# Performance work log

Measured on AMD Instinct MI355X. Metric: run time of the kernel, lower is better.

Reference implementation:

```python
import jax, jax.numpy as jnp
import numpy as np
import math

B, N = 2, 384
TF, POS, TIME = 22, 32, 32
TPROJ = TIME + 1  # embed_fixed appends frame_mask channel
CS, CZ = 256, 128
POS_MAX, TIME_MAX = 2056.0, 10000.0
LN_EPS = 1e-5


def _index_emb(idx):
    # sinusoidal positional embedding of integer indices -> [..., POS]
    K = jnp.arange(POS // 2, dtype=jnp.float32)
    ang = idx[..., None].astype(jnp.float32) * jnp.pi / (POS_MAX ** (2.0 * K / POS))
    return jnp.concatenate([jnp.sin(ang), jnp.cos(ang)], axis=-1)


def _time_emb(t):
    # standard score-sde timestep embedding -> [M, TIME]
    half = TIME // 2
    freqs = jnp.exp(-(math.log(TIME_MAX) / (half - 1)) * jnp.arange(half, dtype=jnp.float32))
    ang = t[:, None] * freqs[None, :]
    return jnp.concatenate([jnp.sin(ang), jnp.cos(ang)], axis=-1)


def _ln(x, g, b):
    m = jnp.mean(x, axis=-1, keepdims=True)
    v = jnp.var(x, axis=-1, keepdims=True)
    return (x - m) * jax.lax.rsqrt(v + LN_EPS) * g + b


def _lin(x, W, b):
    return x @ W.T + b


def _forward(seq_idx, seq_feat, timestep, frame_mask,
             W_npos, b_npos, W_ntf, b_ntf, W_ntime, b_ntime,
             W_n1, b_n1, W_n2, b_n2, g_n, be_n,
             W_epos, b_epos, W_etf, b_etf, W_etime, b_etime,
             W_e1, b_e1, W_e2, b_e2, g_e, be_e):
    Bn, Nn = seq_idx.shape
    rel = seq_idx[:, :, None] - seq_idx[:, None, :]  # [B,N,N]
    seq_emb = _lin(_index_emb(seq_idx), W_npos, b_npos)          # [B,N,CS]
    edge_emb = _lin(_index_emb(rel), W_epos, b_epos)             # [B,N,N,CZ]
    seq_emb = seq_emb + _lin(seq_feat, W_ntf, b_ntf)
    # _cross_concat(x) @ W^T == (x @ Wl^T)[:, :, None] + (x @ Wr^T)[:, None, :] + b
    # (same math, avoids the O(N^2 * 2*TF) concatenated intermediate)
    edge_emb = edge_emb + (seq_feat @ W_etf[:, :TF].T)[:, :, None, :] \
                        + (seq_feat @ W_etf[:, TF:].T)[:, None, :, :] + b_etf
    t_res = (timestep[:, None] * frame_mask).reshape(-1)
    temb = _time_emb(t_res).reshape(Bn, Nn, TIME)
    temb = jnp.concatenate([temb, frame_mask[..., None]], axis=-1)  # embed_fixed -> TPROJ
    seq_emb = seq_emb + _lin(temb, W_ntime, b_ntime)
    edge_emb = edge_emb + (temb @ W_etime[:, :TPROJ].T)[:, :, None, :] \
                        + (temb @ W_etime[:, TPROJ:].T)[:, None, :, :] + b_etime
    # node_embedder: ReLU -> Linear -> ReLU -> Linear -> LayerNorm
    h = _lin(jax.nn.relu(seq_emb), W_n1, b_n1)
    seq_emb = _ln(_lin(jax.nn.relu(h), W_n2, b_n2), g_n, be_n)
    h = _lin(jax.nn.relu(edge_emb), W_e1, b_e1)
    edge_emb = _ln(_lin(jax.nn.relu(h), W_e2, b_e2), g_e, be_e)
    return seq_emb, edge_emb


def setup_inputs() -> dict:
    key = jax.random.key(0)
    ks = jax.random.split(key, 20)
    inp = {
        'seq_idx': jnp.sort(jax.random.randint(ks[0], (B, N), 0, 1000), axis=-1),
        'seq_feat': jax.random.normal(ks[1], (B, N, TF), dtype=jnp.float32),
        'timestep': jax.random.uniform(ks[2], (B,), dtype=jnp.float32),
        'frame_mask': jnp.ones((B, N), dtype=jnp.float32),
    }
    def lin(k, o, i):
        return 0.02 * jax.random.normal(k, (o, i), dtype=jnp.float32), jnp.zeros((o,), jnp.float32)
    inp['W_npos'], inp['b_npos'] = lin(ks[3], CS, POS)
    inp['W_ntf'], inp['b_ntf'] = lin(ks[4], CS, TF)
    inp['W_ntime'], inp['b_ntime'] = lin(ks[5], CS, TPROJ)
    inp['W_n1'], inp['b_n1'] = lin(ks[6], CS, CS)
    inp['W_n2'], inp['b_n2'] = lin(ks[7], CS, CS)
    inp['g_n'], inp['be_n'] = jnp.ones((CS,), jnp.float32), jnp.zeros((CS,), jnp.float32)
    inp['W_epos'], inp['b_epos'] = lin(ks[8], CZ, POS)
    inp['W_etf'], inp['b_etf'] = lin(ks[9], CZ, 2 * TF)
    inp['W_etime'], inp['b_etime'] = lin(ks[10], CZ, 2 * TPROJ)
    inp['W_e1'], inp['b_e1'] = lin(ks[11], CZ, CZ)
    inp['W_e2'], inp['b_e2'] = lin(ks[12], CZ, CZ)
    inp['g_e'], inp['be_e'] = jnp.ones((CZ,), jnp.float32), jnp.zeros((CZ,), jnp.float32)
    return inp


def reference(seq_idx, seq_feat, timestep, frame_mask,
              W_npos, b_npos, W_ntf, b_ntf, W_ntime, b_ntime,
              W_n1, b_n1, W_n2, b_n2, g_n, be_n,
              W_epos, b_epos, W_etf, b_etf, W_etime, b_etime,
              W_e1, b_e1, W_e2, b_e2, g_e, be_e):
    return _forward(seq_idx, seq_feat, timestep, frame_mask,
                    W_npos, b_npos, W_ntf, b_ntf, W_ntime, b_ntime,
                    W_n1, b_n1, W_n2, b_n2, g_n, be_n,
                    W_epos, b_epos, W_etf, b_etf, W_etime, b_etime,
                    W_e1, b_e1, W_e2, b_e2, g_e, be_e)
```

## Files before the change

### kernel.cpp

```cpp
#include <hip/hip_runtime.h>
#include <hip/hip_bf16.h>

#define BB 2
#define NN 384
#define TFD 22
#define POSD 32
#define TPROJ 33
#define CS 256
#define CZ 128
#define PI_F 3.14159265358979323846f

typedef __hip_bfloat16 bf16;
typedef __attribute__((ext_vector_type(8))) short short8;
typedef __attribute__((ext_vector_type(4))) short short4v;
typedef __attribute__((ext_vector_type(4))) float floatx4;

__device__ __forceinline__ float bfbits2f(unsigned short u) {
  unsigned v = ((unsigned)u) << 16;
  float f;
  __builtin_memcpy(&f, &v, 4);
  return f;
}
__device__ __forceinline__ unsigned short f2bf(float x) {
  bf16 h = __float2bfloat16(x);
  unsigned short u;
  __builtin_memcpy(&u, &h, 2);
  return u;
}
__device__ __forceinline__ bool probe_f32(const void* fm) {
  return *(const unsigned*)fm == 0x3F800000u;
}
__device__ __forceinline__ float ldf(const void* p, int j, bool f32) {
  return f32 ? ((const float*)p)[j] : bfbits2f(((const unsigned short*)p)[j]);
}

#define TAB_OFF 0
#define SEQ0_OFF 262144
#define EL_OFF 458752
#define ER_OFF 557056
#define P2_OFF 655360
#define WB_OFF 656896
#define qBN1 0
#define qBN2 256
#define qGN 512
#define qBEN 768
#define qBE1 1024
#define qBE2 1152
#define qGE 1280
#define qBEE 1408
#define UB_WE1 0
#define UB_WE2 16384
#define UB_WN1 32768
#define UB_WN2 98304

#define NODE8_BLKS 96
#define TAB_BLKS 1024
#define CVT_BLKS 646
#define NODE_BLKS 48

struct InPtrs { const void* p[28]; };

__global__ __launch_bounds__(256) void prep(InPtrs ip, const int* __restrict__ seq_idx,
                                            float* __restrict__ ws) {
  const bool f32 = probe_f32(ip.p[3]);
  const int blk = blockIdx.x;
  const int t = threadIdx.x;
  if (blk < NODE8_BLKS) {
    __shared__ float feat[8][88];
    const int bn0 = blk * 8;
    if (t < 128) {
      const int n = t >> 4, j = t & 15, bn = bn0 + n, b = bn / NN;
      const float fm = ldf(ip.p[3], bn, f32);
      const float idxv = (float)seq_idx[bn];
      const float ang = idxv * PI_F * powf(2056.0f, -(float)j * (1.0f / 16.0f));
      feat[n][j] = sinf(ang);
      feat[n][16 + j] = cosf(ang);
      const float tres = ldf(ip.p[2], b, f32) * fm;
      const float freq = expf(-(logf(10000.0f) * (1.0f / 15.0f)) * (float)j);
      feat[n][54 + j] = sinf(tres * freq);
      feat[n][70 + j] = cosf(tres * freq);
      if (j == 0) feat[n][86] = fm;
    }
    if (t < 176) {
      const int n = t / TFD, j = t - n * TFD;
      feat[n][32 + j] = ldf(ip.p[1], (bn0 + n) * TFD + j, f32);
    }
    __syncthreads();
    {
      const int c = t;
      const float bias = ldf(ip.p[5], c, f32) + ldf(ip.p[7], c, f32) + ldf(ip.p[9], c, f32);
      float acc[8];
#pragma unroll
      for (int n = 0; n < 8; ++n) acc[n] = bias;
      if (f32) {
        const float* w = (const float*)ip.p[4] + c * POSD;
#pragma unroll
        for (int k = 0; k < POSD; ++k) { const float wv = w[k];
#pragma unroll
          for (int n = 0; n < 8; ++n) acc[n] += feat[n][k] * wv; }
        const float* w2 = (const float*)ip.p[6] + c * TFD;
#pragma unroll
        for (int k = 0; k < TFD; ++k) { const float wv = w2[k];
#pragma unroll
          for (int n = 0; n < 8; ++n) acc[n] += feat[n][32 + k] * wv; }
        const float* w3 = (const float*)ip.p[8] + c * TPROJ;
#pragma unroll
        for (int k = 0; k < TPROJ; ++k) { const float wv = w3[k];
#pragma unroll
          for (int n = 0; n < 8; ++n) acc[n] += feat[n][54 + k] * wv; }
      } else {
        const unsigned short* w = (const unsigned short*)ip.p[4] + c * POSD;
#pragma unroll
        for (int k = 0; k < POSD; ++k) { const float wv = bfbits2f(w[k]);
#pragma unroll
          for (int n = 0; n < 8; ++n) acc[n] += feat[n][k] * wv; }
        const unsigned short* w2 = (const unsigned short*)ip.p[6] + c * TFD;
#pragma unroll
        for (int k = 0; k < TFD; ++k) { const float wv = bfbits2f(w2[k]);
#pragma unroll
          for (int n = 0; n < 8; ++n) acc[n] += feat[n][32 + k] * wv; }
        const unsigned short* w3 = (const unsigned short*)ip.p[8] + c * TPROJ;
#pragma unroll
        for (int k = 0; k < TPROJ; ++k) { const float wv = bfbits2f(w3[k]);
#pragma unroll
          for (int n = 0; n < 8; ++n) acc[n] += feat[n][54 + k] * wv; }
      }
#pragma unroll
      for (int n = 0; n < 8; ++n) ws[SEQ0_OFF + (bn0 + n) * CS + c] = acc[n];
    }
    {
      const int isR = t >> 7;
      const int c = t & 127;
      const int o1 = isR ? TFD : 0, o2 = isR ? TPROJ : 0;
      const int dst = isR ? ER_OFF : EL_OFF;
      float acc[8];
#pragma unroll
      for (int n = 0; n < 8; ++n) acc[n] = 0.0f;
      if (f32) {
        const float* w = (const float*)ip.p[18] + c * (2 * TFD) + o1;
#pragma unroll
        for (int k = 0; k < TFD; ++k) { const float wv = w[k];
#pragma unroll
          for (int n = 0; n < 8; ++n) acc[n] += feat[n][32 + k] * wv; }
        const float* w2 = (const float*)ip.p[20] + c * (2 * TPROJ) + o2;
#pragma unroll
        for (int k = 0; k < TPROJ; ++k) { const float wv = w2[k];
#pragma unroll
          for (int n = 0; n < 8; ++n) acc[n] += feat[n][54 + k] * wv; }
      } else {
        const unsigned short* w = (const unsigned short*)ip.p[18] + c * (2 * TFD) + o1;
#pragma unroll
        for (int k = 0; k < TFD; ++k) { const float wv = bfbits2f(w[k]);
#pragma unroll
          for (int n = 0; n < 8; ++n) acc[n] += feat[n][32 + k] * wv; }
        const unsigned short* w2 = (const unsigned short*)ip.p[20] + c * (2 * TPROJ) + o2;
#pragma unroll
        for (int k = 0; k < TPROJ; ++k) { const float wv = bfbits2f(w2[k]);
#pragma unroll
          for (int n = 0; n < 8; ++n) acc[n] += feat[n][54 + k] * wv; }
      }
#pragma unroll
      for (int n = 0; n < 8; ++n) ws[dst + (bn0 + n) * CZ + c] = acc[n];
    }
  } else if (blk < NODE8_BLKS + TAB_BLKS) {
    __shared__ float spe[2][POSD];
    const int r0 = (blk - NODE8_BLKS) * 2;
    const int rr = t >> 7, c = t & 127;
    if (c < 16) {
      float ang = (float)(r0 + rr - 1024) * PI_F * powf(2056.0f, -(float)c * (1.0f / 16.0f));
      spe[rr][c] = sinf(ang);
      spe[rr][c + 16] = cosf(ang);
    }
    __syncthreads();
    float acc = ldf(ip.p[17], c, f32) + ldf(ip.p[19], c, f32) + ldf(ip.p[21], c, f32);
    if (f32) {
      const float* w = (const float*)ip.p[16] + c * POSD;
#pragma unroll
      for (int k = 0; k < POSD; ++k) acc += spe[rr][k] * w[k];
    } else {
      const unsigned short* w = (const unsigned short*)ip.p[16] + c * POSD;
#pragma unroll
      for (int k = 0; k < POSD; ++k) acc += spe[rr][k] * bfbits2f(w[k]);
    }
    ws[TAB_OFF + (r0 + rr) * CZ + c] = acc;
  } else {
    const int idx = (blk - NODE8_BLKS - TAB_BLKS) * 256 + t;
    if (idx < 1536) {
      int src, off;
      if (idx < 256)       { src = 11; off = idx; }
      else if (idx < 512)  { src = 13; off = idx - 256; }
      else if (idx < 768)  { src = 14; off = idx - 512; }
      else if (idx < 1024) { src = 15; off = idx - 768; }
      else if (idx < 1152) { src = 23; off = idx - 1024; }
      else if (idx < 1280) { src = 25; off = idx - 1152; }
      else if (idx < 1408) { src = 26; off = idx - 1280; }
      else                 { src = 27; off = idx - 1408; }
      ws[P2_OFF + idx] = ldf(ip.p[src], off, f32);
    } else {
      const int j = idx - 1536;
      int src, loc;
      if (j < 16384)      { src = 22; loc = j; }
      else if (j < 32768) { src = 24; loc = j - 16384; }
      else if (j < 98304) { src = 10; loc = j - 32768; }
      else                { src = 12; loc = j - 98304; }
      const void* sp = ip.p[src];
      unsigned short* wb = (unsigned short*)(ws + WB_OFF);
      wb[j] = f32 ? f2bf(((const float*)sp)[loc]) : ((const unsigned short*)sp)[loc];
    }
  }
}

union SMem {
  struct {
    unsigned short A0[32][CZ + 8];
    unsigned short A1[32][CZ + 8];
    float O[32][CZ + 4];
    int J[NN];
  } e;
  struct {
    unsigned short A0[16][CS + 8];
    unsigned short A1[16][CS + 8];
    float O[16][CS + 4];
    float Red[16][16];
    float RedQ[16][16];
    float Mu[16];
    float Rs[16];
  } n;
};

__global__ __launch_bounds__(256) void main_mfma(const int* __restrict__ seq_idx,
                                                 const float* __restrict__ ws,
                                                 const void* __restrict__ fmraw,
                                                 void* __restrict__ outv) {
  __shared__ __align__(16) SMem sm;
  const int t = threadIdx.x;
  const int wave = t >> 6, lane = t & 63, quad = lane >> 4, l16 = lane & 15;
  const float* P2 = ws + P2_OFF;
  const unsigned short* WB = (const unsigned short*)(ws + WB_OFF);
  const bool f32o = probe_f32(fmraw);

  if (blockIdx.x < NODE_BLKS) {
    const int row0 = blockIdx.x * 16;
    const unsigned short* W1 = WB + UB_WN1;
    const unsigned short* W2 = WB + UB_WN2;
    const float* seq0 = ws + SEQ0_OFF;
#pragma unroll
    for (int r = 0; r < 16; ++r)
      sm.n.A0[r][t] = f2bf(fmaxf(seq0[(row0 + r) * CS + t], 0.0f));
    __syncthreads();
    short8 af[8];
    floatx4 acc[4];
#pragma unroll
    for (int ks = 0; ks < 8; ++ks) af[ks] = *(const short8*)&sm.n.A0[l16][ks * 32 + quad * 8];
#pragma unroll
    for (int n = 0; n < 4; ++n) acc[n] = (floatx4){0.f, 0.f, 0.f, 0.f};
#pragma unroll
    for (int ntl = 0; ntl < 4; ++ntl) {
      const int n0 = wave * 64 + ntl * 16;
#pragma unroll
      for (int ks = 0; ks < 8; ++ks) {
        short8 bfr = *(const short8*)&W1[(n0 + l16) * CS + ks * 32 + quad * 8];
        acc[ntl] = __builtin_amdgcn_mfma_f32_16x16x32_bf16(af[ks], bfr, acc[ntl], 0, 0, 0);
      }
    }
#pragma unroll
    for (int ntl = 0; ntl < 4; ++ntl) {
      const int n0 = wave * 64 + ntl * 16;
      const float b1v = P2[qBN1 + n0 + l16];
#pragma unroll
      for (int i = 0; i < 4; ++i)
        sm.n.A1[quad * 4 + i][n0 + l16] = f2bf(fmaxf(acc[ntl][i] + b1v, 0.0f));
    }
    __syncthreads();
#pragma unroll
    for (int ks = 0; ks < 8; ++ks) af[ks] = *(const short8*)&sm.n.A1[l16][ks * 32 + quad * 8];
#pragma unroll
    for (int n = 0; n < 4; ++n) acc[n] = (floatx4){0.f, 0.f, 0.f, 0.f};
#pragma unroll
    for (int ntl = 0; ntl < 4; ++ntl) {
      const int n0 = wave * 64 + ntl * 16;
#pragma unroll
      for (int ks = 0; ks < 8; ++ks) {
        short8 bfr = *(const short8*)&W2[(n0 + l16) * CS + ks * 32 + quad * 8];
        acc[ntl] = __builtin_amdgcn_mfma_f32_16x16x32_bf16(af[ks], bfr, acc[ntl], 0, 0, 0);
      }
    }
#pragma unroll
    for (int ntl = 0; ntl < 4; ++ntl) {
      const int n0 = wave * 64 + ntl * 16;
      const float b2v = P2[qBN2 + n0 + l16];
#pragma unroll
      for (int i = 0; i < 4; ++i)
        sm.n.O[quad * 4 + i][n0 + l16] = acc[ntl][i] + b2v;
    }
    __syncthreads();
    {
      const int r = t >> 4, seg = t & 15;
      float s = 0.f, q = 0.f;
#pragma unroll
      for (int k = 0; k < 16; ++k) { float v = sm.n.O[r][seg * 16 + k]; s += v; q += v * v; }
      sm.n.Red[r][seg] = s;
      sm.n.RedQ[r][seg] = q;
    }
    __syncthreads();
    if (t < 16) {
      float s = 0.f, q = 0.f;
#pragma unroll
      for (int k = 0; k < 16; ++k) { s += sm.n.Red[t][k]; q += sm.n.RedQ[t][k]; }
      float mu = s * (1.0f / CS);
      float var = q * (1.0f / CS) - mu * mu;
      sm.n.Mu[t] = mu;
      sm.n.Rs[t] = rsqrtf(var + 1e-5f);
    }
    __syncthreads();
    {
      const float g = P2[qGN + t], be = P2[qBEN + t];
      if (f32o) {
        float* o = (float*)outv;
#pragma unroll
        for (int r = 0; r < 16; ++r)
          o[(size_t)(row0 + r) * CS + t] = (sm.n.O[r][t] - sm.n.Mu[r]) * sm.n.Rs[r] * g + be;
      } else {
        bf16* o = (bf16*)outv;
#pragma unroll
        for (int r = 0; r < 16; ++r)
          o[(size_t)(row0 + r) * CS + t] =
              __float2bfloat16((sm.n.O[r][t] - sm.n.Mu[r]) * sm.n.Rs[r] * g + be);
      }
    }
    return;
  }

  const int eb = blockIdx.x - NODE_BLKS;
  const int irow = eb % NN, b = eb / NN;
  const unsigned short* W1 = WB + UB_WE1;
  const unsigned short* W2 = WB + UB_WE2;
  const float* tab = ws + TAB_OFF;
  const float* eL = ws + EL_OFF;
  const float* eR = ws + ER_OFF;
  short8 w1f[2][4], w2f[2][4];
  float b1v[2], b2v[2];
#pragma unroll
  for (int ntl = 0; ntl < 2; ++ntl) {
    const int n0 = (wave * 2 + ntl) * 16;
    b1v[ntl] = P2[qBE1 + n0 + l16];
    b2v[ntl] = P2[qBE2 + n0 + l16];
#pragma unroll
    for (int ks = 0; ks < 4; ++ks) {
      w1f[ntl][ks] = *(const short8*)&W1[(n0 + l16) * CZ + ks * 32 + quad * 8];
      w2f[ntl][ks] = *(const short8*)&W2[(n0 + l16) * CZ + ks * 32 + quad * 8];
    }
  }
  for (int k = t; k < NN; k += 256) sm.e.J[k] = seq_idx[b * NN + k];
  const int idx_i = seq_idx[b * NN + irow];
  const int c4 = (t & 31) * 4;
  const int rg = t >> 5;
  const floatx4 eLv = *(const floatx4*)&eL[(b * NN + irow) * CZ + c4];
  const int lr = t >> 3, lseg = t & 7;
  const size_t base0 = ((size_t)(b * NN + irow) * NN) * CZ;
  __syncthreads();

  for (int jt = 0; jt < NN / 32; ++jt) {
    const int j0 = jt * 32;
#pragma unroll
    for (int rr = 0; rr < 4; ++rr) {
      const int r = rg + rr * 8;
      int rel = idx_i - sm.e.J[j0 + r] + 1024;
      rel = min(max(rel, 0), 2047);
      const floatx4 tv = *(const floatx4*)&tab[rel * CZ + c4];
      const floatx4 ev = *(const floatx4*)&eR[(b * NN + j0 + r) * CZ + c4];
      short4v sv;
      sv[0] = (short)f2bf(fmaxf(tv[0] + ev[0] + eLv[0], 0.0f));
      sv[1] = (short)f2bf(fmaxf(tv[1] + ev[1] + eLv[1], 0.0f));
      sv[2] = (short)f2bf(fmaxf(tv[2] + ev[2] + eLv[2], 0.0f));
      sv[3] = (short)f2bf(fmaxf(tv[3] + ev[3] + eLv[3], 0.0f));
      *(short4v*)&sm.e.A0[r][c4] = sv;
    }
    __syncthreads();
    short8 af[2][4];
    floatx4 acc[2][2];
#pragma unroll
    for (int mt = 0; mt < 2; ++mt)
#pragma unroll
      for (int ks = 0; ks < 4; ++ks)
        af[mt][ks] = *(const short8*)&sm.e.A0[mt * 16 + l16][ks * 32 + quad * 8];
#pragma unroll
    for (int mt = 0; mt < 2; ++mt)
#pragma unroll
      for (int n = 0; n < 2; ++n) acc[mt][n] = (floatx4){0.f, 0.f, 0.f, 0.f};
#pragma unroll
    for (int ntl = 0; ntl < 2; ++ntl)
#pragma unroll
      for (int ks = 0; ks < 4; ++ks) {
        acc[0][ntl] = __builtin_amdgcn_mfma_f32_16x16x32_bf16(af[0][ks], w1f[ntl][ks], acc[0][ntl], 0, 0, 0);
        acc[1][ntl] = __builtin_amdgcn_mfma_f32_16x16x32_bf16(af[1][ks], w1f[ntl][ks], acc[1][ntl], 0, 0, 0);
      }
#pragma unroll
    for (int ntl = 0; ntl < 2; ++ntl) {
      const int n0 = (wave * 2 + ntl) * 16;
#pragma unroll
      for (int mt = 0; mt < 2; ++mt)
#pragma unroll
        for (int i = 0; i < 4; ++i)
          sm.e.A1[mt * 16 + quad * 4 + i][n0 + l16] = f2bf(fmaxf(acc[mt][ntl][i] + b1v[ntl], 0.0f));
    }
    __syncthreads();
#pragma unroll
    for (int mt = 0; mt < 2; ++mt)
#pragma unroll
      for (int ks = 0; ks < 4; ++ks)
        af[mt][ks] = *(const short8*)&sm.e.A1[mt * 16 + l16][ks * 32 + quad * 8];
#pragma unroll
    for (int mt = 0; mt < 2; ++mt)
#pragma unroll
      for (int n = 0; n < 2; ++n) acc[mt][n] = (floatx4){0.f, 0.f, 0.f, 0.f};
#pragma unroll
    for (int ntl = 0; ntl < 2; ++ntl)
#pragma unroll
      for (int ks = 0; ks < 4; ++ks) {
        acc[0][ntl] = __builtin_amdgcn_mfma_f32_16x16x32_bf16(af[0][ks], w2f[ntl][ks], acc[0][ntl], 0, 0, 0);
        acc[1][ntl] = __builtin_amdgcn_mfma_f32_16x16x32_bf16(af[1][ks], w2f[ntl][ks], acc[1][ntl], 0, 0, 0);
      }
#pragma unroll
    for (int ntl = 0; ntl < 2; ++ntl) {
      const int n0 = (wave * 2 + ntl) * 16;
#pragma unroll
      for (int mt = 0; mt < 2; ++mt)
#pragma unroll
        for (int i = 0; i < 4; ++i)
          sm.e.O[mt * 16 + quad * 4 + i][n0 + l16] = acc[mt][ntl][i] + b2v[ntl];
    }
    __syncthreads();
    {
      float s = 0.f, q = 0.f;
      float vals[16];
#pragma unroll
      for (int k = 0; k < 16; ++k) {
        const float v = sm.e.O[lr][lseg * 16 + k];
        vals[k] = v;
        s += v;
        q += v * v;
      }
      s += __shfl_xor(s, 1); q += __shfl_xor(q, 1);
      s += __shfl_xor(s, 2); q += __shfl_xor(q, 2);
      s += __shfl_xor(s, 4); q += __shfl_xor(q, 4);
      const float mu = s * (1.0f / CZ);
      const float rs = rsqrtf(q * (1.0f / CZ) - mu * mu + 1e-5f);
      const int cbase = lseg * 16;
      const size_t obase = base0 + (size_t)(j0 + lr) * CZ + cbase;
      if (f32o) {
        float* o = (float*)outv + (size_t)BB * NN * CS;
#pragma unroll
        for (int h = 0; h < 4; ++h) {
          const floatx4 gq = *(const floatx4*)&P2[qGE + cbase + h * 4];
          const floatx4 bq = *(const floatx4*)&P2[qBEE + cbase + h * 4];
          floatx4 ov;
#pragma unroll
          for (int i = 0; i < 4; ++i) ov[i] = (vals[h * 4 + i] - mu) * rs * gq[i] + bq[i];
          *(floatx4*)&o[obase + h * 4] = ov;
        }
      } else {
        bf16* o = (bf16*)outv + (size_t)BB * NN * CS;
        short8 pk[2];
#pragma unroll
        for (int h = 0; h < 4; ++h) {
          const floatx4 gq = *(const floatx4*)&P2[qGE + cbase + h * 4];
          const floatx4 bq = *(const floatx4*)&P2[qBEE + cbase + h * 4];
#pragma unroll
          for (int i = 0; i < 4; ++i)
            pk[h >> 1][(h & 1) * 4 + i] = (short)f2bf((vals[h * 4 + i] - mu) * rs * gq[i] + bq[i]);
        }
        *(short8*)&o[obase] = pk[0];
        *(short8*)&o[obase + 8] = pk[1];
      }
    }
  }
}

extern "C" void kernel_launch(void* const* d_in, const int* in_sizes, int n_in,
                              void* d_out, int out_size, void* d_ws, size_t ws_size,
                              hipStream_t stream) {
  (void)in_sizes; (void)n_in; (void)out_size; (void)ws_size;
  const int* seq_idx = (const int*)d_in[0];
  float* ws = (float*)d_ws;
  InPtrs ip;
  for (int i = 0; i < 28; ++i) ip.p[i] = d_in[i];
  hipLaunchKernelGGL(prep, dim3(NODE8_BLKS + TAB_BLKS + CVT_BLKS), dim3(256), 0, stream,
                     ip, seq_idx, ws);
  hipLaunchKernelGGL(main_mfma, dim3(NODE_BLKS + BB * NN), dim3(256), 0, stream,
                     seq_idx, ws, d_in[3], d_out);
}
```

Before: 310.5 us.

## Split node/edge kernels and make edge MLP wave-private with register-built A tiles

Splits the combined kernel into a node kernel and a separate edge kernel launch. In the edge kernel each wave now owns its own 32 rows and covers all 128 output columns, so the block-wide syncthreads and shared staging disappear. The ReLU input tiles are built straight into MFMA registers, the hidden activation goes through a small XOR-swizzled per-wave LDS scratch, and LayerNorm is done with in-register shuffles. In exchange, weights are reloaded from global or L2 for every tile instead of kept in registers. Output stores become scalar strided writes rather than 16-byte vectors, and register pressure rises with 16 accumulators.

```diff
diff --git a/kernel.cpp b/kernel.cpp
--- a/kernel.cpp
+++ b/kernel.cpp
@@ -12,7 +12,6 @@
 
 typedef __hip_bfloat16 bf16;
 typedef __attribute__((ext_vector_type(8))) short short8;
-typedef __attribute__((ext_vector_type(4))) short short4v;
 typedef __attribute__((ext_vector_type(4))) float floatx4;
 
 __device__ __forceinline__ float bfbits2f(unsigned short u) {
@@ -210,268 +209,265 @@
   }
 }
 
-union SMem {
-  struct {
-    unsigned short A0[32][CZ + 8];
-    unsigned short A1[32][CZ + 8];
-    float O[32][CZ + 4];
-    int J[NN];
-  } e;
-  struct {
-    unsigned short A0[16][CS + 8];
-    unsigned short A1[16][CS + 8];
-    float O[16][CS + 4];
-    float Red[16][16];
-    float RedQ[16][16];
-    float Mu[16];
-    float Rs[16];
-  } n;
+struct SMemN {
+  unsigned short A0[16][CS + 8];
+  unsigned short A1[16][CS + 8];
+  float O[16][CS + 4];
+  float Red[16][16];
+  float RedQ[16][16];
+  float Mu[16];
+  float Rs[16];
 };
 
-__global__ __launch_bounds__(256) void main_mfma(const int* __restrict__ seq_idx,
-                                                 const float* __restrict__ ws,
+__global__ __launch_bounds__(256) void node_mfma(const float* __restrict__ ws,
                                                  const void* __restrict__ fmraw,
                                                  void* __restrict__ outv) {
-  __shared__ __align__(16) SMem sm;
+  __shared__ __align__(16) SMemN sm;
   const int t = threadIdx.x;
   const int wave = t >> 6, lane = t & 63, quad = lane >> 4, l16 = lane & 15;
   const float* P2 = ws + P2_OFF;
   const unsigned short* WB = (const unsigned short*)(ws + WB_OFF);
   const bool f32o = probe_f32(fmraw);
-
-  if (blockIdx.x < NODE_BLKS) {
-    const int row0 = blockIdx.x * 16;
-    const unsigned short* W1 = WB + UB_WN1;
-    const unsigned short* W2 = WB + UB_WN2;
-    const float* seq0 = ws + SEQ0_OFF;
-#pragma unroll
-    for (int r = 0; r < 16; ++r)
-      sm.n.A0[r][t] = f2bf(fmaxf(seq0[(row0 + r) * CS + t], 0.0f));
-    __syncthreads();
-    short8 af[8];
-    floatx4 acc[4];
-#pragma unroll
-    for (int ks = 0; ks < 8; ++ks) af[ks] = *(const short8*)&sm.n.A0[l16][ks * 32 + quad * 8];
-#pragma unroll
-    for (int n = 0; n < 4; ++n) acc[n] = (floatx4){0.f, 0.f, 0.f, 0.f};
-#pragma unroll
-    for (int ntl = 0; ntl < 4; ++ntl) {
-      const int n0 = wave * 64 + ntl * 16;
-#pragma unroll
-      for (int ks = 0; ks < 8; ++ks) {
-        short8 bfr = *(const short8*)&W1[(n0 + l16) * CS + ks * 32 + quad * 8];
-        acc[ntl] = __builtin_amdgcn_mfma_f32_16x16x32_bf16(af[ks], bfr, acc[ntl], 0, 0, 0);
-      }
-    }
-#pragma unroll
-    for (int ntl = 0; ntl < 4; ++ntl) {
-      const int n0 = wave * 64 + ntl * 16;
-      const float b1v = P2[qBN1 + n0 + l16];
-#pragma unroll
-      for (int i = 0; i < 4; ++i)
-        sm.n.A1[quad * 4 + i][n0 + l16] = f2bf(fmaxf(acc[ntl][i] + b1v, 0.0f));
-    }
-    __syncthreads();
-#pragma unroll
-    for (int ks = 0; ks < 8; ++ks) af[ks] = *(const short8*)&sm.n.A1[l16][ks * 32 + quad * 8];
-#pragma unroll
-    for (int n = 0; n < 4; ++n) acc[n] = (floatx4){0.f, 0.f, 0.f, 0.f};
-#pragma unroll
-    for (int ntl = 0; ntl < 4; ++ntl) {
-      const int n0 = wave * 64 + ntl * 16;
-#pragma unroll
-      for (int ks = 0; ks < 8; ++ks) {
-        short8 bfr = *(const short8*)&W2[(n0 + l16) * CS + ks * 32 + quad * 8];
-        acc[ntl] = __builtin_amdgcn_mfma_f32_16x16x32_bf16(af[ks], bfr, acc[ntl], 0, 0, 0);
-      }
-    }
-#pragma unroll
-    for (int ntl = 0; ntl < 4; ++ntl) {
-      const int n0 = wave * 64 + ntl * 16;
-      const float b2v = P2[qBN2 + n0 + l16];
-#pragma unroll
-      for (int i = 0; i < 4; ++i)
-        sm.n.O[quad * 4 + i][n0 + l16] = acc[ntl][i] + b2v;
-    }
-    __syncthreads();
-    {
-      const int r = t >> 4, seg = t & 15;
-      float s = 0.f, q = 0.f;
-#pragma unroll
-      for (int k = 0; k < 16; ++k) { float v = sm.n.O[r][seg * 16 + k]; s += v; q += v * v; }
-      sm.n.Red[r][seg] = s;
-      sm.n.RedQ[r][seg] = q;
-    }
-    __syncthreads();
-    if (t < 16) {
-      float s = 0.f, q = 0.f;
-#pragma unroll
-      for (int k = 0; k < 16; ++k) { s += sm.n.Red[t][k]; q += sm.n.RedQ[t][k]; }
-      float mu = s * (1.0f / CS);
-      float var = q * (1.0f / CS) - mu * mu;
-      sm.n.Mu[t] = mu;
-      sm.n.Rs[t] = rsqrtf(var + 1e-5f);
-    }
-    __syncthreads();
-    {
-      const float g = P2[qGN + t], be = P2[qBEN + t];
-      if (f32o) {
-        float* o = (float*)outv;
-#pragma unroll
-        for (int r = 0; r < 16; ++r)
-          o[(size_t)(row0 + r) * CS + t] = (sm.n.O[r][t] - sm.n.Mu[r]) * sm.n.Rs[r] * g + be;
-      } else {
-        bf16* o = (bf16*)outv;
-#pragma unroll
-        for (int r = 0; r < 16; ++r)
-          o[(size_t)(row0 + r) * CS + t] =
-              __float2bfloat16((sm.n.O[r][t] - sm.n.Mu[r]) * sm.n.Rs[r] * g + be);
-      }
-    }
-    return;
-  }
-
-  const int eb = blockIdx.x - NODE_BLKS;
-  const int irow = eb % NN, b = eb / NN;
+  const int row0 = blockIdx.x * 16;
+  const unsigned short* W1 = WB + UB_WN1;
+  const unsigned short* W2 = WB + UB_WN2;
+  const float* seq0 = ws + SEQ0_OFF;
+#pragma unroll
+  for (int r = 0; r < 16; ++r)
+    sm.A0[r][t] = f2bf(fmaxf(seq0[(row0 + r) * CS + t], 0.0f));
+  __syncthreads();
+  short8 af[8];
+  floatx4 acc[4];
+#pragma unroll
+  for (int ks = 0; ks < 8; ++ks) af[ks] = *(const short8*)&sm.A0[l16][ks * 32 + quad * 8];
+#pragma unroll
+  for (int n = 0; n < 4; ++n) acc[n] = (floatx4){0.f, 0.f, 0.f, 0.f};
+#pragma unroll
+  for (int ntl = 0; ntl < 4; ++ntl) {
+    const int n0 = wave * 64 + ntl * 16;
+#pragma unroll
+    for (int ks = 0; ks < 8; ++ks) {
+      short8 bfr = *(const short8*)&W1[(n0 + l16) * CS + ks * 32 + quad * 8];
+      acc[ntl] = __builtin_amdgcn_mfma_f32_16x16x32_bf16(af[ks], bfr, acc[ntl], 0, 0, 0);
+    }
+  }
+#pragma unroll
+  for (int ntl = 0; ntl < 4; ++ntl) {
+    const int n0 = wave * 64 + ntl * 16;
+    const float b1v = P2[qBN1 + n0 + l16];
+#pragma unroll
+    for (int i = 0; i < 4; ++i)
+      sm.A1[quad * 4 + i][n0 + l16] = f2bf(fmaxf(acc[ntl][i] + b1v, 0.0f));
+  }
+  __syncthreads();
+#pragma unroll
+  for (int ks = 0; ks < 8; ++ks) af[ks] = *(const short8*)&sm.A1[l16][ks * 32 + quad * 8];
+#pragma unroll
+  for (int n = 0; n < 4; ++n) acc[n] = (floatx4){0.f, 0.f, 0.f, 0.f};
+#pragma unroll
+  for (int ntl = 0; ntl < 4; ++ntl) {
+    const int n0 = wave * 64 + ntl * 16;
+#pragma unroll
+    for (int ks = 0; ks < 8; ++ks) {
+      short8 bfr = *(const short8*)&W2[(n0 + l16) * CS + ks * 32 + quad * 8];
+      acc[ntl] = __builtin_amdgcn_mfma_f32_16x16x32_bf16(af[ks], bfr, acc[ntl], 0, 0, 0);
+    }
+  }
+#pragma unroll
+  for (int ntl = 0; ntl < 4; ++ntl) {
+    const int n0 = wave * 64 + ntl * 16;
+    const float b2v = P2[qBN2 + n0 + l16];
+#pragma unroll
+    for (int i = 0; i < 4; ++i)
+      sm.O[quad * 4 + i][n0 + l16] = acc[ntl][i] + b2v;
+  }
+  __syncthreads();
+  {
+    const int r = t >> 4, seg = t & 15;
+    float s = 0.f, q = 0.f;
+#pragma unroll
+    for (int k = 0; k < 16; ++k) { float v = sm.O[r][seg * 16 + k]; s += v; q += v * v; }
+    sm.Red[r][seg] = s;
+    sm.RedQ[r][seg] = q;
+  }
+  __syncthreads();
+  if (t < 16) {
+    float s = 0.f, q = 0.f;
+#pragma unroll
+    for (int k = 0; k < 16; ++k) { s += sm.Red[t][k]; q += sm.RedQ[t][k]; }
+    float mu = s * (1.0f / CS);
+    float var = q * (1.0f / CS) - mu * mu;
+    sm.Mu[t] = mu;
+    sm.Rs[t] = rsqrtf(var + 1e-5f);
+  }
+  __syncthreads();
+  {
+    const float g = P2[qGN + t], be = P2[qBEN + t];
+    if (f32o) {
+      float* o = (float*)outv;
+#pragma unroll
+      for (int r = 0; r < 16; ++r)
+        o[(size_t)(row0 + r) * CS + t] = (sm.O[r][t] - sm.Mu[r]) * sm.Rs[r] * g + be;
+    } else {
+      bf16* o = (bf16*)outv;
+#pragma unroll
+      for (int r = 0; r < 16; ++r)
+        o[(size_t)(row0 + r) * CS + t] =
+            __float2bfloat16((sm.O[r][t] - sm.Mu[r]) * sm.Rs[r] * g + be);
+    }
+  }
+}
+
+__global__ __launch_bounds__(256) void edge_pw(const int* __restrict__ seq_idx,
+                                               const float* __restrict__ ws,
+                                               const void* __restrict__ fmraw,
+                                               void* __restrict__ outv) {
+  __shared__ __align__(16) unsigned char scrb[4][4096];
+  const int t = threadIdx.x;
+  const int wave = t >> 6, lane = t & 63, quad = lane >> 4, l16 = lane & 15;
+  const float* P2 = ws + P2_OFF;
+  const unsigned short* WB = (const unsigned short*)(ws + WB_OFF);
   const unsigned short* W1 = WB + UB_WE1;
   const unsigned short* W2 = WB + UB_WE2;
   const float* tab = ws + TAB_OFF;
-  const float* eL = ws + EL_OFF;
-  const float* eR = ws + ER_OFF;
-  short8 w1f[2][4], w2f[2][4];
-  float b1v[2], b2v[2];
-#pragma unroll
-  for (int ntl = 0; ntl < 2; ++ntl) {
-    const int n0 = (wave * 2 + ntl) * 16;
-    b1v[ntl] = P2[qBE1 + n0 + l16];
-    b2v[ntl] = P2[qBE2 + n0 + l16];
-#pragma unroll
-    for (int ks = 0; ks < 4; ++ks) {
-      w1f[ntl][ks] = *(const short8*)&W1[(n0 + l16) * CZ + ks * 32 + quad * 8];
-      w2f[ntl][ks] = *(const short8*)&W2[(n0 + l16) * CZ + ks * 32 + quad * 8];
-    }
-  }
-  for (int k = t; k < NN; k += 256) sm.e.J[k] = seq_idx[b * NN + k];
+  const bool f32o = probe_f32(fmraw);
+
+  const int eb = blockIdx.x;
+  const int irow = eb % NN, b = eb / NN;
   const int idx_i = seq_idx[b * NN + irow];
-  const int c4 = (t & 31) * 4;
-  const int rg = t >> 5;
-  const floatx4 eLv = *(const floatx4*)&eL[(b * NN + irow) * CZ + c4];
-  const int lr = t >> 3, lseg = t & 7;
+  const float* el = ws + EL_OFF + (size_t)(b * NN + irow) * CZ;
+  const float* eRb = ws + ER_OFF + (size_t)b * NN * CZ;
   const size_t base0 = ((size_t)(b * NN + irow) * NN) * CZ;
-  __syncthreads();
-
-  for (int jt = 0; jt < NN / 32; ++jt) {
-    const int j0 = jt * 32;
-#pragma unroll
-    for (int rr = 0; rr < 4; ++rr) {
-      const int r = rg + rr * 8;
-      int rel = idx_i - sm.e.J[j0 + r] + 1024;
+  unsigned char* scrw = &scrb[wave][0];
+
+  for (int it = 0; it < 3; ++it) {
+    short8 af[2][4];
+    int jbase[2];
+#pragma unroll
+    for (int mt = 0; mt < 2; ++mt) {
+      const int j0 = (it * 8 + wave * 2 + mt) * 16;
+      jbase[mt] = j0;
+      const int jv = seq_idx[b * NN + j0 + l16];
+      int rel = idx_i - jv + 1024;
       rel = min(max(rel, 0), 2047);
-      const floatx4 tv = *(const floatx4*)&tab[rel * CZ + c4];
-      const floatx4 ev = *(const floatx4*)&eR[(b * NN + j0 + r) * CZ + c4];
-      short4v sv;
-      sv[0] = (short)f2bf(fmaxf(tv[0] + ev[0] + eLv[0], 0.0f));
-      sv[1] = (short)f2bf(fmaxf(tv[1] + ev[1] + eLv[1], 0.0f));
-      sv[2] = (short)f2bf(fmaxf(tv[2] + ev[2] + eLv[2], 0.0f));
-      sv[3] = (short)f2bf(fmaxf(tv[3] + ev[3] + eLv[3], 0.0f));
-      *(short4v*)&sm.e.A0[r][c4] = sv;
-    }
-    __syncthreads();
-    short8 af[2][4];
-    floatx4 acc[2][2];
+      const float* tr = tab + (size_t)rel * CZ;
+      const float* er = eRb + (size_t)(j0 + l16) * CZ;
+#pragma unroll
+      for (int ks = 0; ks < 4; ++ks) {
+        const int c = ks * 32 + quad * 8;
+        const floatx4 t0 = *(const floatx4*)&tr[c];
+        const floatx4 t1 = *(const floatx4*)&tr[c + 4];
+        const floatx4 r0 = *(const floatx4*)&er[c];
+        const floatx4 r1 = *(const floatx4*)&er[c + 4];
+        const floatx4 l0 = *(const floatx4*)&el[c];
+        const floatx4 l1 = *(const floatx4*)&el[c + 4];
+        short8 v;
+#pragma unroll
+        for (int u = 0; u < 4; ++u) v[u] = (short)f2bf(fmaxf(t0[u] + r0[u] + l0[u], 0.0f));
+#pragma unroll
+        for (int u = 0; u < 4; ++u) v[4 + u] = (short)f2bf(fmaxf(t1[u] + r1[u] + l1[u], 0.0f));
+        af[mt][ks] = v;
+      }
+    }
+    floatx4 acc[2][8];
 #pragma unroll
     for (int mt = 0; mt < 2; ++mt)
 #pragma unroll
+      for (int n = 0; n < 8; ++n) acc[mt][n] = (floatx4){0.f, 0.f, 0.f, 0.f};
+#pragma unroll
+    for (int ntl = 0; ntl < 8; ++ntl) {
+      const unsigned short* wrow = W1 + (size_t)(ntl * 16 + l16) * CZ;
+#pragma unroll
+      for (int ks = 0; ks < 4; ++ks) {
+        const short8 bfr = *(const short8*)&wrow[ks * 32 + quad * 8];
+        acc[0][ntl] = __builtin_amdgcn_mfma_f32_16x16x32_bf16(af[0][ks], bfr, acc[0][ntl], 0, 0, 0);
+        acc[1][ntl] = __builtin_amdgcn_mfma_f32_16x16x32_bf16(af[1][ks], bfr, acc[1][ntl], 0, 0, 0);
+      }
+    }
+    short8 af2[2][4];
+#pragma unroll
+    for (int mt = 0; mt < 2; ++mt) {
+#pragma unroll
+      for (int ntl = 0; ntl < 8; ++ntl) {
+        const float b1v = P2[qBE1 + ntl * 16 + l16];
+        const int colb = (ntl * 16 + l16) * 2;
+#pragma unroll
+        for (int i = 0; i < 4; ++i) {
+          const int row = quad * 4 + i;
+          *(unsigned short*)&scrw[row * 256 + (colb ^ ((row & 7) << 4))] =
+              f2bf(fmaxf(acc[mt][ntl][i] + b1v, 0.0f));
+        }
+      }
+#pragma unroll
       for (int ks = 0; ks < 4; ++ks)
-        af[mt][ks] = *(const short8*)&sm.e.A0[mt * 16 + l16][ks * 32 + quad * 8];
+        af2[mt][ks] =
+            *(const short8*)&scrw[l16 * 256 + ((ks * 64 + quad * 16) ^ ((l16 & 7) << 4))];
+    }
 #pragma unroll
     for (int mt = 0; mt < 2; ++mt)
 #pragma unroll
-      for (int n = 0; n < 2; ++n) acc[mt][n] = (floatx4){0.f, 0.f, 0.f, 0.f};
-#pragma unroll
-    for (int ntl = 0; ntl < 2; ++ntl)
+      for (int n = 0; n < 8; ++n) acc[mt][n] = (floatx4){0.f, 0.f, 0.f, 0.f};
+#pragma unroll
+    for (int ntl = 0; ntl < 8; ++ntl) {
+      const unsigned short* wrow = W2 + (size_t)(ntl * 16 + l16) * CZ;
 #pragma unroll
       for (int ks = 0; ks < 4; ++ks) {
-        acc[0][ntl] = __builtin_amdgcn_mfma_f32_16x16x32_bf16(af[0][ks], w1f[ntl][ks], acc[0][ntl], 0, 0, 0);
-        acc[1][ntl] = __builtin_amdgcn_mfma_f32_16x16x32_bf16(af[1][ks], w1f[ntl][ks], acc[1][ntl], 0, 0, 0);
-      }
-#pragma unroll
-    for (int ntl = 0; ntl < 2; ++ntl) {
-      const int n0 = (wave * 2 + ntl) * 16;
-#pragma unroll
-      for (int mt = 0; mt < 2; ++mt)
-#pragma unroll
-        for (int i = 0; i < 4; ++i)
-          sm.e.A1[mt * 16 + quad * 4 + i][n0 + l16] = f2bf(fmaxf(acc[mt][ntl][i] + b1v[ntl], 0.0f));
-    }
-    __syncthreads();
-#pragma unroll
-    for (int mt = 0; mt < 2; ++mt)
-#pragma unroll
-      for (int ks = 0; ks < 4; ++ks)
-        af[mt][ks] = *(const short8*)&sm.e.A1[mt * 16 + l16][ks * 32 + quad * 8];
-#pragma unroll
-    for (int mt = 0; mt < 2; ++mt)
-#pragma unroll
-      for (int n = 0; n < 2; ++n) acc[mt][n] = (floatx4){0.f, 0.f, 0.f, 0.f};
-#pragma unroll
-    for (int ntl = 0; ntl < 2; ++ntl)
-#pragma unroll
-      for (int ks = 0; ks < 4; ++ks) {
-        acc[0][ntl] = __builtin_amdgcn_mfma_f32_16x16x32_bf16(af[0][ks], w2f[ntl][ks], acc[0][ntl], 0, 0, 0);
-        acc[1][ntl] = __builtin_amdgcn_mfma_f32_16x16x32_bf16(af[1][ks], w2f[ntl][ks], acc[1][ntl], 0, 0, 0);
-      }
-#pragma unroll
-    for (int ntl = 0; ntl < 2; ++ntl) {
-      const int n0 = (wave * 2 + ntl) * 16;
-#pragma unroll
-      for (int mt = 0; mt < 2; ++mt)
-#pragma unroll
-        for (int i = 0; i < 4; ++i)
-          sm.e.O[mt * 16 + quad * 4 + i][n0 + l16] = acc[mt][ntl][i] + b2v[ntl];
-    }
-    __syncthreads();
-    {
-      float s = 0.f, q = 0.f;
-      float vals[16];
-#pragma unroll
-      for (int k = 0; k < 16; ++k) {
-        const float v = sm.e.O[lr][lseg * 16 + k];
-        vals[k] = v;
-        s += v;
-        q += v * v;
-      }
-      s += __shfl_xor(s, 1); q += __shfl_xor(q, 1);
-      s += __shfl_xor(s, 2); q += __shfl_xor(q, 2);
-      s += __shfl_xor(s, 4); q += __shfl_xor(q, 4);
-      const float mu = s * (1.0f / CZ);
-      const float rs = rsqrtf(q * (1.0f / CZ) - mu * mu + 1e-5f);
-      const int cbase = lseg * 16;
-      const size_t obase = base0 + (size_t)(j0 + lr) * CZ + cbase;
+        const short8 bfr = *(const short8*)&wrow[ks * 32 + quad * 8];
+        acc[0][ntl] = __builtin_amdgcn_mfma_f32_16x16x32_bf16(af2[0][ks], bfr, acc[0][ntl], 0, 0, 0);
+        acc[1][ntl] = __builtin_amdgcn_mfma_f32_16x16x32_bf16(af2[1][ks], bfr, acc[1][ntl], 0, 0, 0);
+      }
+    }
+#pragma unroll
+    for (int mt = 0; mt < 2; ++mt) {
+      float s[4] = {0.f, 0.f, 0.f, 0.f}, q[4] = {0.f, 0.f, 0.f, 0.f};
+#pragma unroll
+      for (int ntl = 0; ntl < 8; ++ntl) {
+        const float b2v = P2[qBE2 + ntl * 16 + l16];
+#pragma unroll
+        for (int i = 0; i < 4; ++i) {
+          const float v = acc[mt][ntl][i] + b2v;
+          acc[mt][ntl][i] = v;
+          s[i] += v;
+          q[i] += v * v;
+        }
+      }
+#pragma unroll
+      for (int m = 1; m <= 8; m <<= 1) {
+#pragma unroll
+        for (int i = 0; i < 4; ++i) {
+          s[i] += __shfl_xor(s[i], m);
+          q[i] += __shfl_xor(q[i], m);
+        }
+      }
+      float mu[4], rs[4];
+#pragma unroll
+      for (int i = 0; i < 4; ++i) {
+        mu[i] = s[i] * (1.0f / CZ);
+        rs[i] = rsqrtf(q[i] * (1.0f / CZ) - mu[i] * mu[i] + 1e-5f);
+      }
+      const int j0 = jbase[mt];
       if (f32o) {
         float* o = (float*)outv + (size_t)BB * NN * CS;
 #pragma unroll
-        for (int h = 0; h < 4; ++h) {
-          const floatx4 gq = *(const floatx4*)&P2[qGE + cbase + h * 4];
-          const floatx4 bq = *(const floatx4*)&P2[qBEE + cbase + h * 4];
-          floatx4 ov;
-#pragma unroll
-          for (int i = 0; i < 4; ++i) ov[i] = (vals[h * 4 + i] - mu) * rs * gq[i] + bq[i];
-          *(floatx4*)&o[obase + h * 4] = ov;
+        for (int ntl = 0; ntl < 8; ++ntl) {
+          const float g = P2[qGE + ntl * 16 + l16];
+          const float be = P2[qBEE + ntl * 16 + l16];
+#pragma unroll
+          for (int i = 0; i < 4; ++i)
+            o[base0 + (size_t)(j0 + quad * 4 + i) * CZ + ntl * 16 + l16] =
+                (acc[mt][ntl][i] - mu[i]) * rs[i] * g + be;
         }
       } else {
         bf16* o = (bf16*)outv + (size_t)BB * NN * CS;
-        short8 pk[2];
-#pragma unroll
-        for (int h = 0; h < 4; ++h) {
-          const floatx4 gq = *(const floatx4*)&P2[qGE + cbase + h * 4];
-          const floatx4 bq = *(const floatx4*)&P2[qBEE + cbase + h * 4];
+#pragma unroll
+        for (int ntl = 0; ntl < 8; ++ntl) {
+          const float g = P2[qGE + ntl * 16 + l16];
+          const float be = P2[qBEE + ntl * 16 + l16];
 #pragma unroll
           for (int i = 0; i < 4; ++i)
-            pk[h >> 1][(h & 1) * 4 + i] = (short)f2bf((vals[h * 4 + i] - mu) * rs * gq[i] + bq[i]);
+            o[base0 + (size_t)(j0 + quad * 4 + i) * CZ + ntl * 16 + l16] =
+                __float2bfloat16((acc[mt][ntl][i] - mu[i]) * rs[i] * g + be);
         }
-        *(short8*)&o[obase] = pk[0];
-        *(short8*)&o[obase + 8] = pk[1];
       }
     }
   }
@@ -487,6 +483,6 @@
   for (int i = 0; i < 28; ++i) ip.p[i] = d_in[i];
   hipLaunchKernelGGL(prep, dim3(NODE8_BLKS + TAB_BLKS + CVT_BLKS), dim3(256), 0, stream,
                      ip, seq_idx, ws);
-  hipLaunchKernelGGL(main_mfma, dim3(NODE_BLKS + BB * NN), dim3(256), 0, stream,
-                     seq_idx, ws, d_in[3], d_out);
-}
+  hipLaunchKernelGGL(node_mfma, dim3(NODE_BLKS), dim3(256), 0, stream, ws, d_in[3], d_out);
+  hipLaunchKernelGGL(edge_pw, dim3(BB * NN), dim3(256), 0, stream, seq_idx, ws, d_in[3], d_out);
+}
```

Result: slower. 335.4 us (+8.0%).
